# Kernel optimization log

Hardware: AMD Instinct MI355X
Metric: run time of the kernel (lower is better)

## Reference

```python
import jax, jax.numpy as jnp
import numpy as np

B, L, D = 16384, 5, 1024  # batch, lesionNum, feat_dim == att_dim
LN_EPS = 1e-5


def _layernorm(x, g, b):
    mu = jnp.mean(x, axis=-1, keepdims=True)
    var = jnp.var(x, axis=-1, keepdims=True)
    return (x - mu) * jax.lax.rsqrt(var + LN_EPS) * g + b


def setup_inputs() -> dict:
    key = jax.random.key(0)
    ks = jax.random.split(key, 8)
    s = 0.02
    x = jax.random.normal(ks[0], (B, L, D), dtype=jnp.float32)
    mask = jax.random.randint(ks[1], (1, L), 0, 2, dtype=jnp.int64)
    mask = mask.at[0, 0].set(1)  # guarantee at least one unmasked position
    Wq = jax.random.normal(ks[2], (D, D), dtype=jnp.float32) * s
    Wk = jax.random.normal(ks[3], (D, D), dtype=jnp.float32) * s
    Wv = jax.random.normal(ks[4], (D, D), dtype=jnp.float32) * s
    W1 = jax.random.normal(ks[5], (D, D), dtype=jnp.float32) * s
    b1 = jnp.zeros((D,), dtype=jnp.float32)
    W2 = jax.random.normal(ks[6], (D, D), dtype=jnp.float32) * s
    b2 = jnp.zeros((D,), dtype=jnp.float32)
    att_g = jnp.ones((D,), dtype=jnp.float32)
    att_b = jnp.zeros((D,), dtype=jnp.float32)
    ff_g = jnp.ones((D,), dtype=jnp.float32)
    ff_b = jnp.zeros((D,), dtype=jnp.float32)
    return dict(x=x, mask=mask, Wq=Wq, Wk=Wk, Wv=Wv, W1=W1, b1=b1, W2=W2,
                b2=b2, att_g=att_g, att_b=att_b, ff_g=ff_g, ff_b=ff_b)


def reference(x, mask, Wq, Wk, Wv, W1, b1, W2, b2, att_g, att_b, ff_g, ff_b):
    # QKV (no bias). With nhead=1 the reshape makes scores per-token dot
    # products: (B,L,1,D) @ (B,L,D,1) -> (B,L,1,1); we keep them as (B,L).
    q = jnp.einsum('bld,ed->ble', x, Wq)
    k = jnp.einsum('bld,ed->ble', x, Wk)
    v = jnp.einsum('bld,ed->ble', x, Wv)
    scores = jnp.sum(q * k, axis=-1) / jnp.sqrt(jnp.float32(D))  # (B,L)
    # torch loop sets -inf where ANY mask row has 0 (applied to all batches)
    keep = jnp.all(mask != 0, axis=0)  # (L,)
    scores = jnp.where(keep[None, :], scores, -jnp.inf)
    probs = jax.nn.softmax(scores, axis=1)  # softmax over token dim (dim=1)
    probs = jnp.where(jnp.isnan(probs), 0.0, probs)  # nan-safe (all-masked)
    attn = probs[:, :, None] * v  # (B,L,1,1)@(B,L,1,D) == per-token scaling
    y = _layernorm(attn + x, att_g, att_b)
    # FFN: Linear -> exact GELU -> Linear (dropout inactive in eval)
    h = jax.nn.gelu(jnp.einsum('bld,ed->ble', y, W1) + b1, approximate=False)
    ff = jnp.einsum('bld,ed->ble', h, W2) + b2
    return _layernorm(ff + y, ff_g, ff_b)
```

## Files before the change

kernel.cpp:

```cpp
#include <hip/hip_runtime.h>
#include <hip/hip_bf16.h>
#include <cstdint>


typedef float f32x4 __attribute__((ext_vector_type(4)));
typedef __bf16 bf16x8 __attribute__((ext_vector_type(8)));

#define DD 1024
#define NROWS 81920L

__device__ __forceinline__ unsigned short f2bf(float f) {
  union { float f; unsigned u; } c; c.f = f;
  unsigned u = c.u;
  return (unsigned short)((u + 0x7FFFu + ((u >> 16) & 1u)) >> 16);
}
__device__ __forceinline__ float bf2f(unsigned short b) {
  union { unsigned u; float f; } c; c.u = ((unsigned)b) << 16;
  return c.f;
}
__device__ __forceinline__ void unpack8(uint4 v, float* o) {
  o[0] = bf2f((unsigned short)(v.x & 0xffffu)); o[1] = bf2f((unsigned short)(v.x >> 16));
  o[2] = bf2f((unsigned short)(v.y & 0xffffu)); o[3] = bf2f((unsigned short)(v.y >> 16));
  o[4] = bf2f((unsigned short)(v.z & 0xffffu)); o[5] = bf2f((unsigned short)(v.z >> 16));
  o[6] = bf2f((unsigned short)(v.w & 0xffffu)); o[7] = bf2f((unsigned short)(v.w >> 16));
}
__device__ __forceinline__ void gload_lds16(const void* g, void* l) {
  __builtin_amdgcn_global_load_lds(
      (const __attribute__((address_space(1))) unsigned int*)g,
      (__attribute__((address_space(3))) unsigned int*)l, 16, 0, 0);
}

__global__ void __launch_bounds__(256) k_cvt_bf16(const float* __restrict__ in,
                                                  unsigned short* __restrict__ out, long n) {
  long i = ((long)blockIdx.x * blockDim.x + threadIdx.x) * 8;
  long stride = (long)gridDim.x * blockDim.x * 8;
  for (; i < n; i += stride) {
    f32x4 a = *(const f32x4*)(in + i);
    f32x4 b = *(const f32x4*)(in + i + 4);
    uint4 o;
    o.x = (unsigned)f2bf(a[0]) | ((unsigned)f2bf(a[1]) << 16);
    o.y = (unsigned)f2bf(a[2]) | ((unsigned)f2bf(a[3]) << 16);
    o.z = (unsigned)f2bf(b[0]) | ((unsigned)f2bf(b[1]) << 16);
    o.w = (unsigned)f2bf(b[2]) | ((unsigned)f2bf(b[3]) << 16);
    *(uint4*)(out + i) = o;
  }
}

__global__ void __launch_bounds__(256) k_gt(const float* __restrict__ Wq,
                                            const float* __restrict__ Wk,
                                            unsigned short* __restrict__ Gt) {
  __shared__ float sk[16][16];
  __shared__ float sq[16][64];
  const int tx = threadIdx.x, ty = threadIdx.y;
  const int n0 = blockIdx.y * 16;
  const int k0 = blockIdx.x * 64;
  float acc[4] = {0.f, 0.f, 0.f, 0.f};
  for (int e0 = 0; e0 < 1024; e0 += 16) {
    sk[ty][tx] = Wk[(long)(e0 + ty) * DD + n0 + tx];
    *(f32x4*)&sq[ty][tx * 4] = *(const f32x4*)&Wq[(long)(e0 + ty) * DD + k0 + tx * 4];
    __syncthreads();
#pragma unroll
    for (int ee = 0; ee < 16; ++ee) {
      float kv = sk[ee][ty];
      f32x4 qv = *(const f32x4*)&sq[ee][tx * 4];
      acc[0] += kv * qv[0]; acc[1] += kv * qv[1];
      acc[2] += kv * qv[2]; acc[3] += kv * qv[3];
    }
    __syncthreads();
  }
  uint2 o;
  o.x = (unsigned)f2bf(acc[0]) | ((unsigned)f2bf(acc[1]) << 16);
  o.y = (unsigned)f2bf(acc[2]) | ((unsigned)f2bf(acc[3]) << 16);
  *(uint2*)&Gt[(long)(n0 + ty) * DD + k0 + tx * 4] = o;
}


#define PHASE(BUFC, KK, MIH, DOSTAGE, STG_ISB, STG_KK, SN, TRAILV)             \
  {                                                                            \
    const char* rb_ = (BUFC) + ((KK) << 14);                                   \
    if ((MIH) == 0) {                                                          \
      _Pragma("unroll") for (int j = 0; j < 4; ++j)                            \
        fb[j] = *(const bf16x8*)(rb_ + boff[j]);                               \
      _Pragma("unroll") for (int i = 0; i < 4; ++i)                            \
        fa[i] = *(const bf16x8*)(rb_ + aoff[i]);                               \
    } else {                                                                   \
      _Pragma("unroll") for (int i = 0; i < 4; ++i)                            \
        fa[i] = *(const bf16x8*)(rb_ + aoff[4 + i]);                           \
    }                                                                          \
    if (DOSTAGE) {                                                             \
      if (STG_ISB) stageB((SN), (STG_KK)); else stageA((SN), (STG_KK));        \
    }                                                                          \
    __builtin_amdgcn_s_barrier();                                              \
    asm volatile("s_waitcnt lgkmcnt(0)" ::: "memory");                         \
    __builtin_amdgcn_sched_barrier(0);                                         \
    __builtin_amdgcn_s_setprio(1);                                             \
    _Pragma("unroll") for (int i = 0; i < 4; ++i)                              \
      _Pragma("unroll") for (int j = 0; j < 4; ++j)                            \
        acc[(MIH) * 4 + i][j] = __builtin_amdgcn_mfma_f32_16x16x32_bf16(       \
            fa[i], fb[j], acc[(MIH) * 4 + i][j], 0, 0, 0);                     \
    __builtin_amdgcn_s_setprio(0);                                             \
    if ((TRAILV) == 1) asm volatile("s_waitcnt vmcnt(4)" ::: "memory");        \
    else if ((TRAILV) == 2) asm volatile("s_waitcnt vmcnt(0)" ::: "memory");   \
    __builtin_amdgcn_s_barrier();                                              \
    asm volatile("" ::: "memory");                                             \
  }

template <int EPI>
__global__ void __launch_bounds__(512, 2) k_gemm256(
    const unsigned short* __restrict__ A,
    const unsigned short* __restrict__ B,
    unsigned short* __restrict__ outb,
    float* __restrict__ outf,
    const float* __restrict__ bias,
    const unsigned short* __restrict__ resid,
    const int ntl2,
    const int cst) {
  __shared__ __align__(16) char ldsB[131072];
  const int tid = threadIdx.x;
  const int lane = tid & 63;
  const int wid = tid >> 6;
  const int wm = wid >> 2, wn = wid & 3;

  const int nwg = gridDim.x;
  const int cpx = nwg >> 3;
  const int dd = blockIdx.x;
  const int lgc = (dd & 7) * cpx + (dd >> 3);
  const int mt = lgc >> ntl2;
  const int nt = lgc & ((1 << ntl2) - 1);
  const long m0 = (long)mt * 256;
  const int n0 = nt * 256;

  const int q = tid >> 2;
  const int gcol = (((tid & 3) ^ ((q >> 1) & 3)) << 4);
  const char* gA = (const char*)A + (m0 + q) * 2048 + gcol;
  const char* gB = (const char*)B + ((long)n0 + q) * 2048 + gcol;
  const int ldst = tid * 16;

  auto stageA = [&](int s, int kk) {
    char* dst = ldsB + ((s & 1) << 16) + (kk << 14) + ldst;
    const char* src = gA + (long)s * 128 + (kk << 6);
    gload_lds16(src, dst);
    gload_lds16(src + 128 * 2048, dst + 8192);
  };
  auto stageB = [&](int s, int kk) {
    char* dst = ldsB + ((s & 1) << 16) + 32768 + (kk << 14) + ldst;
    const char* src = gB + (long)s * 128 + (kk << 6);
    gload_lds16(src, dst);
    gload_lds16(src + 128 * 2048, dst + 8192);
  };

  const int la = lane & 15, lg = lane >> 4;
  const int cb = ((lg ^ ((la >> 1) & 3)) << 4);
  int aoff[8], boff[4];
#pragma unroll
  for (int mi = 0; mi < 8; ++mi) aoff[mi] = (wm * 128 + mi * 16 + la) * 64 + cb;
#pragma unroll
  for (int nj = 0; nj < 4; ++nj) boff[nj] = 32768 + (wn * 64 + nj * 16 + la) * 64 + cb;

  f32x4 acc[8][4];
#pragma unroll
  for (int mi = 0; mi < 8; ++mi)
#pragma unroll
    for (int nj = 0; nj < 4; ++nj) acc[mi][nj] = f32x4{0.f, 0.f, 0.f, 0.f};

  bf16x8 fa[4], fb[4];

  stageA(0, 0); stageB(0, 0); stageA(0, 1); stageB(0, 1);
  asm volatile("s_waitcnt vmcnt(4)" ::: "memory");
  __builtin_amdgcn_s_barrier();
  asm volatile("" ::: "memory");

  for (int s = 0; s < 15; ++s) {
    const int sn = s + 1;
    char* bufc = ldsB + ((s & 1) << 16);
    PHASE(bufc, 0, 0, true, false, 0, sn, 0);
    PHASE(bufc, 0, 1, true, true,  0, sn, 1);
    PHASE(bufc, 1, 0, true, false, 1, sn, 0);
    PHASE(bufc, 1, 1, true, true,  1, sn, 1);
  }
  {
    char* bufc = ldsB + ((15 & 1) << 16);
    PHASE(bufc, 0, 0, false, false, 0, 16, 0);
    PHASE(bufc, 0, 1, false, false, 0, 16, 2);
    PHASE(bufc, 1, 0, false, false, 1, 16, 0);
    PHASE(bufc, 1, 1, false, false, 1, 16, 0);
  }

  const long rbase = m0 + wm * 128 + (lane >> 4) * 4;
  const int cbase = n0 + wn * 64 + la;
#pragma unroll
  for (int mi = 0; mi < 8; ++mi) {
#pragma unroll
    for (int nj = 0; nj < 4; ++nj) {
      const int col = cbase + nj * 16;
      float bv = 0.f;
      if constexpr (EPI != 0) bv = bias[col];
#pragma unroll
      for (int t = 0; t < 4; ++t) {
        const long r = rbase + mi * 16 + t;
        float v = acc[mi][nj][t];
        if constexpr (EPI == 0) {
          outb[r * (long)cst + col] = f2bf(v);
        } else if constexpr (EPI == 1) {
          v += bv;
          v = 0.5f * v * (1.0f + erff(v * 0.70710678118654752f));
          outb[r * (long)cst + col] = f2bf(v);
        } else if constexpr (EPI == 2) {
          v += bv + bf2f(resid[r * (long)cst + col]);
          outf[r * (long)cst + col] = v;
        } else {
          v += bv + bf2f(resid[r * (long)cst + col]);
          outb[r * (long)cst + col] = f2bf(v);
        }
      }
    }
  }
}

__global__ void __launch_bounds__(256) k_attn_ln(
    const unsigned short* __restrict__ xb, const unsigned short* __restrict__ uv,
    unsigned short* __restrict__ yb, const int* __restrict__ mask,
    const float* __restrict__ att_g, const float* __restrict__ att_b) {
  const int b = blockIdx.x * 4 + (threadIdx.x >> 6);
  const int lane = threadIdx.x & 63;
  const long xbase = (long)b * 5120 + lane * 16;
  const long ubase = (long)b * 10240 + lane * 16;

  float xr[5][16];
  float sc[5];
#pragma unroll
  for (int l = 0; l < 5; ++l) {
    const unsigned short* xp = xb + xbase + l * 1024;
    const unsigned short* up = uv + ubase + l * 2048;
    unpack8(*(const uint4*)xp, xr[l]); unpack8(*(const uint4*)(xp + 8), xr[l] + 8);
    float uu[16];
    unpack8(*(const uint4*)up, uu); unpack8(*(const uint4*)(up + 8), uu + 8);
    float d = 0.f;
#pragma unroll
    for (int c = 0; c < 16; ++c) d += xr[l][c] * uu[c];
#pragma unroll
    for (int off = 32; off; off >>= 1) d += __shfl_xor(d, off);
    sc[l] = d * 0.03125f;
  }
  bool keep[5];
  float m = -1e30f;
#pragma unroll
  for (int l = 0; l < 5; ++l) {
    keep[l] = (mask[l] != 0);
    if (keep[l]) m = fmaxf(m, sc[l]);
  }
  float p[5], s = 0.f;
#pragma unroll
  for (int l = 0; l < 5; ++l) {
    p[l] = keep[l] ? __expf(sc[l] - m) : 0.f;
    s += p[l];
  }
  const float inv = 1.f / s;

  float gg[16], bb[16];
  {
    const float* gp = att_g + lane * 16;
    const float* bp = att_b + lane * 16;
#pragma unroll
    for (int q = 0; q < 4; ++q) {
      f32x4 gv = *(const f32x4*)(gp + q * 4);
      f32x4 bv = *(const f32x4*)(bp + q * 4);
#pragma unroll
      for (int c = 0; c < 4; ++c) { gg[q * 4 + c] = gv[c]; bb[q * 4 + c] = bv[c]; }
    }
  }

#pragma unroll
  for (int l = 0; l < 5; ++l) {
    const unsigned short* vp = uv + ubase + l * 2048 + 1024;
    float vv[16];
    unpack8(*(const uint4*)vp, vv); unpack8(*(const uint4*)(vp + 8), vv + 8);
    const float pl = p[l] * inv;
    float t[16], sm = 0.f, sq = 0.f;
#pragma unroll
    for (int c = 0; c < 16; ++c) {
      t[c] = pl * vv[c] + xr[l][c];
      sm += t[c];
      sq += t[c] * t[c];
    }
#pragma unroll
    for (int off = 32; off; off >>= 1) {
      sm += __shfl_xor(sm, off);
      sq += __shfl_xor(sq, off);
    }
    const float mu = sm * (1.f / 1024.f);
    const float var = sq * (1.f / 1024.f) - mu * mu;
    const float rs = rsqrtf(var + 1e-5f);
    unsigned short r[16];
#pragma unroll
    for (int c = 0; c < 16; ++c) r[c] = f2bf((t[c] - mu) * rs * gg[c] + bb[c]);
    uint4 o0, o1;
    o0.x = (unsigned)r[0] | ((unsigned)r[1] << 16);  o0.y = (unsigned)r[2] | ((unsigned)r[3] << 16);
    o0.z = (unsigned)r[4] | ((unsigned)r[5] << 16);  o0.w = (unsigned)r[6] | ((unsigned)r[7] << 16);
    o1.x = (unsigned)r[8] | ((unsigned)r[9] << 16);  o1.y = (unsigned)r[10] | ((unsigned)r[11] << 16);
    o1.z = (unsigned)r[12] | ((unsigned)r[13] << 16); o1.w = (unsigned)r[14] | ((unsigned)r[15] << 16);
    unsigned short* yp = yb + xbase + l * 1024;
    *(uint4*)yp = o0;
    *(uint4*)(yp + 8) = o1;
  }
}

__global__ void __launch_bounds__(256) k_ln_final_bf(const unsigned short* __restrict__ zb,
                                                     float* __restrict__ out,
                                                     const float* __restrict__ g,
                                                     const float* __restrict__ bb) {
  const int lane = threadIdx.x & 63;
  const long row = (long)blockIdx.x * 4 + (threadIdx.x >> 6);
  const unsigned short* p = zb + row * DD + lane * 16;
  float t[16];
  unpack8(*(const uint4*)p, t);
  unpack8(*(const uint4*)(p + 8), t + 8);
  float sm = 0.f, sq = 0.f;
#pragma unroll
  for (int c = 0; c < 16; ++c) { sm += t[c]; sq += t[c] * t[c]; }
#pragma unroll
  for (int off = 32; off; off >>= 1) {
    sm += __shfl_xor(sm, off);
    sq += __shfl_xor(sq, off);
  }
  const float mu = sm * (1.f / 1024.f);
  const float var = sq * (1.f / 1024.f) - mu * mu;
  const float rs = rsqrtf(var + 1e-5f);
  float* op = out + row * DD + lane * 16;
  const float* gp = g + lane * 16;
  const float* bp = bb + lane * 16;
#pragma unroll
  for (int q = 0; q < 4; ++q) {
    f32x4 gv = *(const f32x4*)(gp + q * 4);
    f32x4 bv = *(const f32x4*)(bp + q * 4);
    f32x4 o;
#pragma unroll
    for (int c = 0; c < 4; ++c) o[c] = (t[q * 4 + c] - mu) * rs * gv[c] + bv[c];
    *(f32x4*)(op + q * 4) = o;
  }
}

__global__ void __launch_bounds__(256) k_ln_final(float* __restrict__ z,
                                                  const float* __restrict__ g,
                                                  const float* __restrict__ bb) {
  const int lane = threadIdx.x & 63;
  const long row = (long)blockIdx.x * 4 + (threadIdx.x >> 6);
  float* p = z + row * DD + lane * 16;
  f32x4 v[4];
  float sm = 0.f, sq = 0.f;
#pragma unroll
  for (int q = 0; q < 4; ++q) {
    v[q] = *(const f32x4*)(p + q * 4);
#pragma unroll
    for (int c = 0; c < 4; ++c) { sm += v[q][c]; sq += v[q][c] * v[q][c]; }
  }
#pragma unroll
  for (int off = 32; off; off >>= 1) {
    sm += __shfl_xor(sm, off);
    sq += __shfl_xor(sq, off);
  }
  const float mu = sm * (1.f / 1024.f);
  const float var = sq * (1.f / 1024.f) - mu * mu;
  const float rs = rsqrtf(var + 1e-5f);
  const float* gp = g + lane * 16;
  const float* bp = bb + lane * 16;
#pragma unroll
  for (int q = 0; q < 4; ++q) {
    f32x4 gv = *(const f32x4*)(gp + q * 4);
    f32x4 bv = *(const f32x4*)(bp + q * 4);
#pragma unroll
    for (int c = 0; c < 4; ++c) v[q][c] = (v[q][c] - mu) * rs * gv[c] + bv[c];
    *(f32x4*)(p + q * 4) = v[q];
  }
}

extern "C" void kernel_launch(void* const* d_in, const int* in_sizes, int n_in,
                              void* d_out, int out_size, void* d_ws, size_t ws_size,
                              hipStream_t stream) {
  const float* x     = (const float*)d_in[0];
  const int*   mask  = (const int*)d_in[1];
  const float* Wq    = (const float*)d_in[2];
  const float* Wk    = (const float*)d_in[3];
  const float* Wv    = (const float*)d_in[4];
  const float* W1    = (const float*)d_in[5];
  const float* b1    = (const float*)d_in[6];
  const float* W2    = (const float*)d_in[7];
  const float* b2    = (const float*)d_in[8];
  const float* att_g = (const float*)d_in[9];
  const float* att_b = (const float*)d_in[10];
  const float* ff_g  = (const float*)d_in[11];
  const float* ff_b  = (const float*)d_in[12];

  const long NE = NROWS * DD;
  unsigned short* xb   = (unsigned short*)d_ws;
  unsigned short* hb   = xb + NE;
  unsigned short* Bcat = hb + NE;
  unsigned short* W1b  = Bcat + 2L * DD * DD;
  unsigned short* W2b  = W1b + (long)DD * DD;
  unsigned short* zb   = W2b + (long)DD * DD;

  const size_t need_zb = (size_t)(3L * NE + 4L * DD * DD) * 2;
  const bool use_zb = ws_size >= need_zb;

  unsigned short* uvb = (unsigned short*)d_out;
  float* outf = (float*)d_out;

  k_cvt_bf16<<<2048, 256, 0, stream>>>(x, xb, NE);
  k_cvt_bf16<<<512, 256, 0, stream>>>(Wv, Bcat + (long)DD * DD, (long)DD * DD);
  k_cvt_bf16<<<512, 256, 0, stream>>>(W1, W1b, (long)DD * DD);
  k_cvt_bf16<<<512, 256, 0, stream>>>(W2, W2b, (long)DD * DD);
  k_gt<<<dim3(16, 64), dim3(16, 16), 0, stream>>>(Wq, Wk, Bcat);

  k_gemm256<0><<<2560, 512, 0, stream>>>(xb, Bcat, uvb, nullptr, nullptr, nullptr, 3, 2048);
  k_attn_ln<<<4096, 256, 0, stream>>>(xb, uvb, xb, mask, att_g, att_b);
  k_gemm256<1><<<1280, 512, 0, stream>>>(xb, W1b, hb, nullptr, b1, nullptr, 2, 1024);
  if (use_zb) {
    k_gemm256<3><<<1280, 512, 0, stream>>>(hb, W2b, zb, nullptr, b2, xb, 2, 1024);
    k_ln_final_bf<<<20480, 256, 0, stream>>>(zb, outf, ff_g, ff_b);
  } else {
    k_gemm256<2><<<1280, 512, 0, stream>>>(hb, W2b, nullptr, outf, b2, xb, 2, 1024);
    k_ln_final<<<20480, 256, 0, stream>>>(outf, ff_g, ff_b);
  }
}
```

Measured before the change: 1.247 ms.

## Add 128x256 triple-buffered GEMM for FFN and merge conversion kernels

Adds a new GEMM kernel with 128x256 tiles and a three-stage LDS pipeline (one barrier per k-step) for the two 1024x1024 FFN GEMMs. This doubles the workgroup count to 2560 for better CU load balance and latency hiding. It also merges the four fp32-to-bf16 conversion launches into one kernel to cut launch overhead. The smaller tile gives less operand reuse per workgroup, which raises global and L2 traffic.

Result: slower. 1.293 ms (+3.7%).

```diff
diff --git a/kernel.cpp b/kernel.cpp
--- a/kernel.cpp
+++ b/kernel.cpp
@@ -29,20 +29,32 @@
       (const __attribute__((address_space(1))) unsigned int*)g,
       (__attribute__((address_space(3))) unsigned int*)l, 16, 0, 0);
 }
-
-__global__ void __launch_bounds__(256) k_cvt_bf16(const float* __restrict__ in,
-                                                  unsigned short* __restrict__ out, long n) {
+__device__ __forceinline__ void cvt8(const float* src, unsigned short* dst, long i) {
+  f32x4 a = *(const f32x4*)(src + i);
+  f32x4 b = *(const f32x4*)(src + i + 4);
+  uint4 o;
+  o.x = (unsigned)f2bf(a[0]) | ((unsigned)f2bf(a[1]) << 16);
+  o.y = (unsigned)f2bf(a[2]) | ((unsigned)f2bf(a[3]) << 16);
+  o.z = (unsigned)f2bf(b[0]) | ((unsigned)f2bf(b[1]) << 16);
+  o.w = (unsigned)f2bf(b[2]) | ((unsigned)f2bf(b[3]) << 16);
+  *(uint4*)(dst + i) = o;
+}
+
+__global__ void __launch_bounds__(256) k_cvt_multi(
+    const float* __restrict__ x, const float* __restrict__ Wv,
+    const float* __restrict__ W1, const float* __restrict__ W2,
+    unsigned short* __restrict__ xb, unsigned short* __restrict__ wvb,
+    unsigned short* __restrict__ w1b, unsigned short* __restrict__ w2b) {
+  const long NE = NROWS * DD;
+  const long M2 = (long)DD * DD;
+  const long total = NE + 3 * M2;
   long i = ((long)blockIdx.x * blockDim.x + threadIdx.x) * 8;
-  long stride = (long)gridDim.x * blockDim.x * 8;
-  for (; i < n; i += stride) {
-    f32x4 a = *(const f32x4*)(in + i);
-    f32x4 b = *(const f32x4*)(in + i + 4);
-    uint4 o;
-    o.x = (unsigned)f2bf(a[0]) | ((unsigned)f2bf(a[1]) << 16);
-    o.y = (unsigned)f2bf(a[2]) | ((unsigned)f2bf(a[3]) << 16);
-    o.z = (unsigned)f2bf(b[0]) | ((unsigned)f2bf(b[1]) << 16);
-    o.w = (unsigned)f2bf(b[2]) | ((unsigned)f2bf(b[3]) << 16);
-    *(uint4*)(out + i) = o;
+  const long stride = (long)gridDim.x * blockDim.x * 8;
+  for (; i < total; i += stride) {
+    if (i < NE) cvt8(x, xb, i);
+    else if (i < NE + M2) cvt8(Wv, wvb, i - NE);
+    else if (i < NE + 2 * M2) cvt8(W1, w1b, i - NE - M2);
+    else cvt8(W2, w2b, i - NE - 2 * M2);
   }
 }
 
@@ -73,7 +85,6 @@
   o.y = (unsigned)f2bf(acc[2]) | ((unsigned)f2bf(acc[3]) << 16);
   *(uint2*)&Gt[(long)(n0 + ty) * DD + k0 + tx * 4] = o;
 }
-
 
 #define PHASE(BUFC, KK, MIH, DOSTAGE, STG_ISB, STG_KK, SN, TRAILV)             \
   {                                                                            \
@@ -110,11 +121,7 @@
     const unsigned short* __restrict__ A,
     const unsigned short* __restrict__ B,
     unsigned short* __restrict__ outb,
-    float* __restrict__ outf,
-    const float* __restrict__ bias,
-    const unsigned short* __restrict__ resid,
-    const int ntl2,
-    const int cst) {
+    const int ntl2, const int cst) {
   __shared__ __align__(16) char ldsB[131072];
   const int tid = threadIdx.x;
   const int lane = tid & 63;
@@ -189,28 +196,128 @@
   const long rbase = m0 + wm * 128 + (lane >> 4) * 4;
   const int cbase = n0 + wn * 64 + la;
 #pragma unroll
-  for (int mi = 0; mi < 8; ++mi) {
+  for (int mi = 0; mi < 8; ++mi)
 #pragma unroll
     for (int nj = 0; nj < 4; ++nj) {
       const int col = cbase + nj * 16;
-      float bv = 0.f;
-      if constexpr (EPI != 0) bv = bias[col];
 #pragma unroll
       for (int t = 0; t < 4; ++t) {
         const long r = rbase + mi * 16 + t;
-        float v = acc[mi][nj][t];
-        if constexpr (EPI == 0) {
-          outb[r * (long)cst + col] = f2bf(v);
-        } else if constexpr (EPI == 1) {
-          v += bv;
+        outb[r * (long)cst + col] = f2bf(acc[mi][nj][t]);
+      }
+    }
+}
+
+#define STEP128(RBUF, S, DOSTAGE, TAILV)                                       \
+  {                                                                            \
+    const char* bA_ = lds3 + (RBUF) * 24576;                                   \
+    const char* bB_ = bA_ + 8192;                                              \
+    bf16x8 fa[4], fb[4];                                                       \
+    _Pragma("unroll") for (int i = 0; i < 4; ++i)                              \
+      fa[i] = *(const bf16x8*)(bA_ + aoff[i]);                                 \
+    _Pragma("unroll") for (int j = 0; j < 4; ++j)                              \
+      fb[j] = *(const bf16x8*)(bB_ + boff[j]);                                 \
+    if (DOSTAGE) stage((S) + 2, lds3 + (((S) + 2) % 3) * 24576);               \
+    __builtin_amdgcn_s_setprio(1);                                             \
+    _Pragma("unroll") for (int i = 0; i < 4; ++i)                              \
+      _Pragma("unroll") for (int j = 0; j < 4; ++j)                            \
+        acc[i][j] = __builtin_amdgcn_mfma_f32_16x16x32_bf16(                   \
+            fa[i], fb[j], acc[i][j], 0, 0, 0);                                 \
+    __builtin_amdgcn_s_setprio(0);                                             \
+    if ((TAILV) == 1) asm volatile("s_waitcnt vmcnt(3)" ::: "memory");         \
+    else if ((TAILV) == 2) asm volatile("s_waitcnt vmcnt(0)" ::: "memory");    \
+    if ((TAILV) != 3) {                                                        \
+      __builtin_amdgcn_s_barrier();                                            \
+      asm volatile("" ::: "memory");                                           \
+    }                                                                          \
+  }
+
+template <int EPI>
+__global__ void __launch_bounds__(512, 2) k_gemm128(
+    const unsigned short* __restrict__ A,
+    const unsigned short* __restrict__ B,
+    unsigned short* __restrict__ outb,
+    float* __restrict__ outf,
+    const float* __restrict__ bias,
+    const unsigned short* __restrict__ resid) {
+  __shared__ __align__(16) char lds3[73728];
+  const int tid = threadIdx.x;
+  const int lane = tid & 63;
+  const int wid = tid >> 6;
+  const int wm = wid >> 2, wn = wid & 3;
+
+  const int nwg = gridDim.x;
+  const int cpx = nwg >> 3;
+  const int dd = blockIdx.x;
+  const int lgc = (dd & 7) * cpx + (dd >> 3);
+  const int mt = lgc >> 2;
+  const int nt = lgc & 3;
+  const long m0 = (long)mt * 128;
+  const int n0 = nt * 256;
+
+  const int q = tid >> 2;
+  const int gcol = (((tid & 3) ^ ((q >> 1) & 3)) << 4);
+  const char* gA = (const char*)A + (m0 + q) * 2048 + gcol;
+  const char* gB = (const char*)B + ((long)n0 + q) * 2048 + gcol;
+  const int ldst = tid * 16;
+
+  auto stage = [&](int s, char* base) {
+    const char* sa = gA + (long)s * 64;
+    const char* sb = gB + (long)s * 64;
+    gload_lds16(sa, base + ldst);
+    gload_lds16(sb, base + 8192 + ldst);
+    gload_lds16(sb + 128 * 2048, base + 16384 + ldst);
+  };
+
+  const int la = lane & 15, lg = lane >> 4;
+  const int cb = ((lg ^ ((la >> 1) & 3)) << 4);
+  int aoff[4], boff[4];
+#pragma unroll
+  for (int mi = 0; mi < 4; ++mi) aoff[mi] = (wm * 64 + mi * 16 + la) * 64 + cb;
+#pragma unroll
+  for (int nj = 0; nj < 4; ++nj) boff[nj] = (wn * 64 + nj * 16 + la) * 64 + cb;
+
+  f32x4 acc[4][4];
+#pragma unroll
+  for (int mi = 0; mi < 4; ++mi)
+#pragma unroll
+    for (int nj = 0; nj < 4; ++nj) acc[mi][nj] = f32x4{0.f, 0.f, 0.f, 0.f};
+
+  stage(0, lds3);
+  stage(1, lds3 + 24576);
+  asm volatile("s_waitcnt vmcnt(3)" ::: "memory");
+  __builtin_amdgcn_s_barrier();
+  asm volatile("" ::: "memory");
+
+  for (int st = 0; st < 30; st += 3) {
+    STEP128(0, st + 0, true, 1);
+    STEP128(1, st + 1, true, 1);
+    STEP128(2, st + 2, true, 1);
+  }
+  STEP128(0, 30, false, 2);
+  STEP128(1, 31, false, 3);
+
+  const long rbase = m0 + wm * 64 + (lane >> 4) * 4;
+  const int cbase = n0 + wn * 64 + la;
+#pragma unroll
+  for (int mi = 0; mi < 4; ++mi) {
+#pragma unroll
+    for (int nj = 0; nj < 4; ++nj) {
+      const int col = cbase + nj * 16;
+      const float bv = bias[col];
+#pragma unroll
+      for (int t = 0; t < 4; ++t) {
+        const long r = rbase + mi * 16 + t;
+        float v = acc[mi][nj][t] + bv;
+        if constexpr (EPI == 1) {
           v = 0.5f * v * (1.0f + erff(v * 0.70710678118654752f));
-          outb[r * (long)cst + col] = f2bf(v);
+          outb[r * (long)DD + col] = f2bf(v);
         } else if constexpr (EPI == 2) {
-          v += bv + bf2f(resid[r * (long)cst + col]);
-          outf[r * (long)cst + col] = v;
+          v += bf2f(resid[r * (long)DD + col]);
+          outf[r * (long)DD + col] = v;
         } else {
-          v += bv + bf2f(resid[r * (long)cst + col]);
-          outb[r * (long)cst + col] = f2bf(v);
+          v += bf2f(resid[r * (long)DD + col]);
+          outb[r * (long)DD + col] = f2bf(v);
         }
       }
     }
@@ -405,20 +512,18 @@
   unsigned short* uvb = (unsigned short*)d_out;
   float* outf = (float*)d_out;
 
-  k_cvt_bf16<<<2048, 256, 0, stream>>>(x, xb, NE);
-  k_cvt_bf16<<<512, 256, 0, stream>>>(Wv, Bcat + (long)DD * DD, (long)DD * DD);
-  k_cvt_bf16<<<512, 256, 0, stream>>>(W1, W1b, (long)DD * DD);
-  k_cvt_bf16<<<512, 256, 0, stream>>>(W2, W2b, (long)DD * DD);
+  k_cvt_multi<<<2048, 256, 0, stream>>>(x, Wv, W1, W2,
+                                        xb, Bcat + (long)DD * DD, W1b, W2b);
   k_gt<<<dim3(16, 64), dim3(16, 16), 0, stream>>>(Wq, Wk, Bcat);
 
-  k_gemm256<0><<<2560, 512, 0, stream>>>(xb, Bcat, uvb, nullptr, nullptr, nullptr, 3, 2048);
+  k_gemm256<0><<<2560, 512, 0, stream>>>(xb, Bcat, uvb, 3, 2048);
   k_attn_ln<<<4096, 256, 0, stream>>>(xb, uvb, xb, mask, att_g, att_b);
-  k_gemm256<1><<<1280, 512, 0, stream>>>(xb, W1b, hb, nullptr, b1, nullptr, 2, 1024);
+  k_gemm128<1><<<2560, 512, 0, stream>>>(xb, W1b, hb, nullptr, b1, nullptr);
   if (use_zb) {
-    k_gemm256<3><<<1280, 512, 0, stream>>>(hb, W2b, zb, nullptr, b2, xb, 2, 1024);
+    k_gemm128<3><<<2560, 512, 0, stream>>>(hb, W2b, zb, nullptr, b2, xb);
     k_ln_final_bf<<<20480, 256, 0, stream>>>(zb, outf, ff_g, ff_b);
   } else {
-    k_gemm256<2><<<1280, 512, 0, stream>>>(hb, W2b, nullptr, outf, b2, xb, 2, 1024);
+    k_gemm128<2><<<2560, 512, 0, stream>>>(hb, W2b, nullptr, outf, b2, xb);
     k_ln_final<<<20480, 256, 0, stream>>>(outf, ff_g, ff_b);
   }
 }
```

## Replace 256x256 LDS GEMM with 128x128 tiles streaming B from global

Applied to the files above, without the earlier changes.

The GEMM moves from 256x256 tiles with 512 threads, where both A and B are staged in LDS, to 128x128 tiles with 256 threads. Only A goes through a triple-buffered LDS ring, and each wave loads its B fragments directly from global memory into registers. The smaller tile and LDS footprint should allow more resident workgroups and fewer barriers, at the cost of less data reuse per tile and more global or L2 traffic for B. The four fp32-to-bf16 conversion launches are also merged into a single kernel.

Measured after the change: 1.920 ms (median of 3 runs). 54.0% more time.

```diff
diff --git a/kernel.cpp b/kernel.cpp
--- a/kernel.cpp
+++ b/kernel.cpp
@@ -29,20 +29,32 @@
       (const __attribute__((address_space(1))) unsigned int*)g,
       (__attribute__((address_space(3))) unsigned int*)l, 16, 0, 0);
 }
-
-__global__ void __launch_bounds__(256) k_cvt_bf16(const float* __restrict__ in,
-                                                  unsigned short* __restrict__ out, long n) {
+__device__ __forceinline__ void cvt8(const float* src, unsigned short* dst, long i) {
+  f32x4 a = *(const f32x4*)(src + i);
+  f32x4 b = *(const f32x4*)(src + i + 4);
+  uint4 o;
+  o.x = (unsigned)f2bf(a[0]) | ((unsigned)f2bf(a[1]) << 16);
+  o.y = (unsigned)f2bf(a[2]) | ((unsigned)f2bf(a[3]) << 16);
+  o.z = (unsigned)f2bf(b[0]) | ((unsigned)f2bf(b[1]) << 16);
+  o.w = (unsigned)f2bf(b[2]) | ((unsigned)f2bf(b[3]) << 16);
+  *(uint4*)(dst + i) = o;
+}
+
+__global__ void __launch_bounds__(256) k_cvt_multi(
+    const float* __restrict__ x, const float* __restrict__ Wv,
+    const float* __restrict__ W1, const float* __restrict__ W2,
+    unsigned short* __restrict__ xb, unsigned short* __restrict__ wvb,
+    unsigned short* __restrict__ w1b, unsigned short* __restrict__ w2b) {
+  const long NE = NROWS * DD;
+  const long M2 = (long)DD * DD;
+  const long total = NE + 3 * M2;
   long i = ((long)blockIdx.x * blockDim.x + threadIdx.x) * 8;
-  long stride = (long)gridDim.x * blockDim.x * 8;
-  for (; i < n; i += stride) {
-    f32x4 a = *(const f32x4*)(in + i);
-    f32x4 b = *(const f32x4*)(in + i + 4);
-    uint4 o;
-    o.x = (unsigned)f2bf(a[0]) | ((unsigned)f2bf(a[1]) << 16);
-    o.y = (unsigned)f2bf(a[2]) | ((unsigned)f2bf(a[3]) << 16);
-    o.z = (unsigned)f2bf(b[0]) | ((unsigned)f2bf(b[1]) << 16);
-    o.w = (unsigned)f2bf(b[2]) | ((unsigned)f2bf(b[3]) << 16);
-    *(uint4*)(out + i) = o;
+  const long stride = (long)gridDim.x * blockDim.x * 8;
+  for (; i < total; i += stride) {
+    if (i < NE) cvt8(x, xb, i);
+    else if (i < NE + M2) cvt8(Wv, wvb, i - NE);
+    else if (i < NE + 2 * M2) cvt8(W1, w1b, i - NE - M2);
+    else cvt8(W2, w2b, i - NE - 2 * M2);
   }
 }
 
@@ -74,39 +86,31 @@
   *(uint2*)&Gt[(long)(n0 + ty) * DD + k0 + tx * 4] = o;
 }
 
-
-#define PHASE(BUFC, KK, MIH, DOSTAGE, STG_ISB, STG_KK, SN, TRAILV)             \
+#define STEPBL(RS, SS, S, DOSTAGE, TAILK)                                      \
   {                                                                            \
-    const char* rb_ = (BUFC) + ((KK) << 14);                                   \
-    if ((MIH) == 0) {                                                          \
-      _Pragma("unroll") for (int j = 0; j < 4; ++j)                            \
-        fb[j] = *(const bf16x8*)(rb_ + boff[j]);                               \
-      _Pragma("unroll") for (int i = 0; i < 4; ++i)                            \
-        fa[i] = *(const bf16x8*)(rb_ + aoff[i]);                               \
-    } else {                                                                   \
-      _Pragma("unroll") for (int i = 0; i < 4; ++i)                            \
-        fa[i] = *(const bf16x8*)(rb_ + aoff[4 + i]);                           \
-    }                                                                          \
-    if (DOSTAGE) {                                                             \
-      if (STG_ISB) stageB((SN), (STG_KK)); else stageA((SN), (STG_KK));        \
-    }                                                                          \
-    __builtin_amdgcn_s_barrier();                                              \
-    asm volatile("s_waitcnt lgkmcnt(0)" ::: "memory");                         \
-    __builtin_amdgcn_sched_barrier(0);                                         \
+    _Pragma("unroll") for (int nj = 0; nj < 4; ++nj)                           \
+      fb[nj] = *(const bf16x8*)(gBw + nj * 32768 + (long)(S) * 64);            \
+    const char* bA_ = ldsA + (RS) * 8192;                                      \
+    bf16x8 fa[4];                                                              \
+    _Pragma("unroll") for (int i = 0; i < 4; ++i)                              \
+      fa[i] = *(const bf16x8*)(bA_ + aoff[i]);                                 \
+    if (DOSTAGE) stageA((S) + 2, ldsA + (SS) * 8192);                          \
     __builtin_amdgcn_s_setprio(1);                                             \
     _Pragma("unroll") for (int i = 0; i < 4; ++i)                              \
       _Pragma("unroll") for (int j = 0; j < 4; ++j)                            \
-        acc[(MIH) * 4 + i][j] = __builtin_amdgcn_mfma_f32_16x16x32_bf16(       \
-            fa[i], fb[j], acc[(MIH) * 4 + i][j], 0, 0, 0);                     \
+        acc[i][j] = __builtin_amdgcn_mfma_f32_16x16x32_bf16(                   \
+            fa[i], fb[j], acc[i][j], 0, 0, 0);                                 \
     __builtin_amdgcn_s_setprio(0);                                             \
-    if ((TRAILV) == 1) asm volatile("s_waitcnt vmcnt(4)" ::: "memory");        \
-    else if ((TRAILV) == 2) asm volatile("s_waitcnt vmcnt(0)" ::: "memory");   \
-    __builtin_amdgcn_s_barrier();                                              \
-    asm volatile("" ::: "memory");                                             \
+    if ((TAILK) == 0) asm volatile("s_waitcnt vmcnt(2)" ::: "memory");         \
+    else if ((TAILK) == 1) asm volatile("s_waitcnt vmcnt(0)" ::: "memory");    \
+    if ((TAILK) != 2) {                                                        \
+      __builtin_amdgcn_s_barrier();                                            \
+      asm volatile("" ::: "memory");                                           \
+    }                                                                          \
   }
 
 template <int EPI>
-__global__ void __launch_bounds__(512, 2) k_gemm256(
+__global__ void __launch_bounds__(256, 4) k_gemm_bl(
     const unsigned short* __restrict__ A,
     const unsigned short* __restrict__ B,
     unsigned short* __restrict__ outb,
@@ -115,11 +119,11 @@
     const unsigned short* __restrict__ resid,
     const int ntl2,
     const int cst) {
-  __shared__ __align__(16) char ldsB[131072];
+  __shared__ __align__(16) char ldsA[24576];
   const int tid = threadIdx.x;
   const int lane = tid & 63;
   const int wid = tid >> 6;
-  const int wm = wid >> 2, wn = wid & 3;
+  const int wm = wid >> 1, wn = wid & 1;
 
   const int nwg = gridDim.x;
   const int cpx = nwg >> 3;
@@ -127,69 +131,54 @@
   const int lgc = (dd & 7) * cpx + (dd >> 3);
   const int mt = lgc >> ntl2;
   const int nt = lgc & ((1 << ntl2) - 1);
-  const long m0 = (long)mt * 256;
-  const int n0 = nt * 256;
+  const long m0 = (long)mt * 128;
+  const int n0 = nt * 128;
 
   const int q = tid >> 2;
-  const int gcol = (((tid & 3) ^ ((q >> 1) & 3)) << 4);
-  const char* gA = (const char*)A + (m0 + q) * 2048 + gcol;
-  const char* gB = (const char*)B + ((long)n0 + q) * 2048 + gcol;
+  const int gcolA = (((tid & 3) ^ ((q >> 1) & 3)) << 4);
+  const char* gA = (const char*)A + (m0 + q) * 2048 + gcolA;
   const int ldst = tid * 16;
 
-  auto stageA = [&](int s, int kk) {
-    char* dst = ldsB + ((s & 1) << 16) + (kk << 14) + ldst;
-    const char* src = gA + (long)s * 128 + (kk << 6);
-    gload_lds16(src, dst);
-    gload_lds16(src + 128 * 2048, dst + 8192);
-  };
-  auto stageB = [&](int s, int kk) {
-    char* dst = ldsB + ((s & 1) << 16) + 32768 + (kk << 14) + ldst;
-    const char* src = gB + (long)s * 128 + (kk << 6);
-    gload_lds16(src, dst);
-    gload_lds16(src + 128 * 2048, dst + 8192);
+  auto stageA = [&](int s, char* base) {
+    const char* src = gA + (long)s * 64;
+    gload_lds16(src, base + ldst);
+    gload_lds16(src + 64 * 2048, base + 4096 + ldst);
   };
 
   const int la = lane & 15, lg = lane >> 4;
   const int cb = ((lg ^ ((la >> 1) & 3)) << 4);
-  int aoff[8], boff[4];
-#pragma unroll
-  for (int mi = 0; mi < 8; ++mi) aoff[mi] = (wm * 128 + mi * 16 + la) * 64 + cb;
-#pragma unroll
-  for (int nj = 0; nj < 4; ++nj) boff[nj] = 32768 + (wn * 64 + nj * 16 + la) * 64 + cb;
-
-  f32x4 acc[8][4];
-#pragma unroll
-  for (int mi = 0; mi < 8; ++mi)
+  int aoff[4];
+#pragma unroll
+  for (int mi = 0; mi < 4; ++mi) aoff[mi] = (wm * 64 + mi * 16 + la) * 64 + cb;
+
+  const char* gBw = (const char*)B + ((long)(n0 + wn * 64 + la) << 11) + (lg << 4);
+
+  f32x4 acc[4][4];
+#pragma unroll
+  for (int mi = 0; mi < 4; ++mi)
 #pragma unroll
     for (int nj = 0; nj < 4; ++nj) acc[mi][nj] = f32x4{0.f, 0.f, 0.f, 0.f};
 
-  bf16x8 fa[4], fb[4];
-
-  stageA(0, 0); stageB(0, 0); stageA(0, 1); stageB(0, 1);
-  asm volatile("s_waitcnt vmcnt(4)" ::: "memory");
+  bf16x8 fb[4];
+
+  stageA(0, ldsA);
+  stageA(1, ldsA + 8192);
+  asm volatile("s_waitcnt vmcnt(2)" ::: "memory");
   __builtin_amdgcn_s_barrier();
   asm volatile("" ::: "memory");
 
-  for (int s = 0; s < 15; ++s) {
-    const int sn = s + 1;
-    char* bufc = ldsB + ((s & 1) << 16);
-    PHASE(bufc, 0, 0, true, false, 0, sn, 0);
-    PHASE(bufc, 0, 1, true, true,  0, sn, 1);
-    PHASE(bufc, 1, 0, true, false, 1, sn, 0);
-    PHASE(bufc, 1, 1, true, true,  1, sn, 1);
-  }
-  {
-    char* bufc = ldsB + ((15 & 1) << 16);
-    PHASE(bufc, 0, 0, false, false, 0, 16, 0);
-    PHASE(bufc, 0, 1, false, false, 0, 16, 2);
-    PHASE(bufc, 1, 0, false, false, 1, 16, 0);
-    PHASE(bufc, 1, 1, false, false, 1, 16, 0);
-  }
-
-  const long rbase = m0 + wm * 128 + (lane >> 4) * 4;
+  for (int t = 0; t < 30; t += 3) {
+    STEPBL(0, 2, t + 0, true, 0);
+    STEPBL(1, 0, t + 1, true, 0);
+    STEPBL(2, 1, t + 2, true, 0);
+  }
+  STEPBL(0, 2, 30, false, 1);
+  STEPBL(1, 0, 31, false, 2);
+
+  const long rbase = m0 + wm * 64 + (lane >> 4) * 4;
   const int cbase = n0 + wn * 64 + la;
 #pragma unroll
-  for (int mi = 0; mi < 8; ++mi) {
+  for (int mi = 0; mi < 4; ++mi) {
 #pragma unroll
     for (int nj = 0; nj < 4; ++nj) {
       const int col = cbase + nj * 16;
@@ -405,20 +394,18 @@
   unsigned short* uvb = (unsigned short*)d_out;
   float* outf = (float*)d_out;
 
-  k_cvt_bf16<<<2048, 256, 0, stream>>>(x, xb, NE);
-  k_cvt_bf16<<<512, 256, 0, stream>>>(Wv, Bcat + (long)DD * DD, (long)DD * DD);
-  k_cvt_bf16<<<512, 256, 0, stream>>>(W1, W1b, (long)DD * DD);
-  k_cvt_bf16<<<512, 256, 0, stream>>>(W2, W2b, (long)DD * DD);
+  k_cvt_multi<<<2048, 256, 0, stream>>>(x, Wv, W1, W2,
+                                        xb, Bcat + (long)DD * DD, W1b, W2b);
   k_gt<<<dim3(16, 64), dim3(16, 16), 0, stream>>>(Wq, Wk, Bcat);
 
-  k_gemm256<0><<<2560, 512, 0, stream>>>(xb, Bcat, uvb, nullptr, nullptr, nullptr, 3, 2048);
+  k_gemm_bl<0><<<10240, 256, 0, stream>>>(xb, Bcat, uvb, nullptr, nullptr, nullptr, 4, 2048);
   k_attn_ln<<<4096, 256, 0, stream>>>(xb, uvb, xb, mask, att_g, att_b);
-  k_gemm256<1><<<1280, 512, 0, stream>>>(xb, W1b, hb, nullptr, b1, nullptr, 2, 1024);
+  k_gemm_bl<1><<<5120, 256, 0, stream>>>(xb, W1b, hb, nullptr, b1, nullptr, 3, 1024);
   if (use_zb) {
-    k_gemm256<3><<<1280, 512, 0, stream>>>(hb, W2b, zb, nullptr, b2, xb, 2, 1024);
+    k_gemm_bl<3><<<5120, 256, 0, stream>>>(hb, W2b, zb, nullptr, b2, xb, 3, 1024);
     k_ln_final_bf<<<20480, 256, 0, stream>>>(zb, outf, ff_g, ff_b);
   } else {
-    k_gemm256<2><<<1280, 512, 0, stream>>>(hb, W2b, nullptr, outf, b2, xb, 2, 1024);
+    k_gemm_bl<2><<<5120, 256, 0, stream>>>(hb, W2b, nullptr, outf, b2, xb, 3, 1024);
     k_ln_final<<<20480, 256, 0, stream>>>(outf, ff_g, ff_b);
   }
 }
```
